# Performance work log

Hardware: AMD Instinct MI355X
Metric: run time of the kernel (lower is better)

The kernel has to match this reference:

```python
import jax, jax.numpy as jnp
import numpy as np

B_, L_, D_, H_ = 2, 1024, 1024, 16


def _matrixR(L, d_model):
    # Transformer-XL sinusoid table, reversed along the position axis (reverse=True)
    inv_freq = 1.0 / (10000.0 ** (np.arange(0, d_model, 2, dtype=np.float32) / d_model))
    sinus = np.arange(L, dtype=np.float32)[:, None] * inv_freq[None, :]
    mat = np.zeros((L, d_model), dtype=np.float32)
    mat[:, 0::2] = np.sin(sinus)
    mat[:, 1::2] = np.cos(sinus)
    return jnp.asarray(mat[::-1].copy())


def _shift_b(x):
    # x: (b, h, L, L) -> TXL relative shift + lower-triangular mask
    b, h, L, _ = x.shape
    pad = jnp.concatenate([jnp.zeros((b, h, L, 1), x.dtype), x], axis=-1)  # (b,h,L,L+1)
    shifted = pad.reshape(b, h, L + 1, L)[:, :, 1:, :]                      # (b,h,L,L)
    return jnp.tril(shifted)


def setup_inputs() -> dict:
    key = jax.random.key(0)
    ks = jax.random.split(key, 8)
    s = 1.0 / np.sqrt(D_)
    return {
        "E": jax.random.normal(ks[0], (B_, L_, D_), dtype=jnp.float32),
        "Ev": jax.random.normal(ks[1], (B_, L_, D_), dtype=jnp.float32),
        "R": _matrixR(L_, D_),
        "Wq": jax.random.normal(ks[2], (D_, D_), dtype=jnp.float32) * s,
        "Wke": jax.random.normal(ks[3], (D_, D_), dtype=jnp.float32) * s,
        "Wkr": jax.random.normal(ks[4], (D_, D_), dtype=jnp.float32) * s,
        "Wv": jax.random.normal(ks[5], (D_, D_), dtype=jnp.float32) * s,
        "cb": jnp.ones((D_,), dtype=jnp.float32),
        "pb": jnp.ones((D_,), dtype=jnp.float32),
        "Wo_w": jax.random.normal(ks[6], (D_, D_), dtype=jnp.float32) * s,
        "Wo_b": jnp.zeros((D_,), dtype=jnp.float32),
        "ln_g": jnp.ones((D_,), dtype=jnp.float32),
        "ln_b": jnp.zeros((D_,), dtype=jnp.float32),
    }


def reference(E, Ev, R, Wq, Wke, Wkr, Wv, cb, pb, Wo_w, Wo_b, ln_g, ln_b):
    b, L, d = E.shape
    h = H_
    dh = d // h
    # projections -> (b, h, L, dh)
    q = (E @ Wq).reshape(b, L, h, dh).transpose(0, 2, 1, 3)
    k = (Ev @ Wke).reshape(b, L, h, dh).transpose(0, 2, 1, 3)
    v = (Ev @ Wv).reshape(b, L, h, dh).transpose(0, 2, 1, 3)
    # relative-position keys (batch independent): (h, L, dh)
    Q = (R @ Wkr).reshape(L, h, dh).transpose(1, 0, 2)
    # (a) content-content
    A_a = jnp.einsum('bhid,bhjd->bhij', q, k)
    # (b) content-position, with shift trick
    A_b = _shift_b(jnp.einsum('bhid,hjd->bhij', q, Q))
    # (c) global content bias (same for every query row)
    A_c = jnp.einsum('hd,bhjd->bhj', cb.reshape(h, dh), k)[:, :, None, :]  # (b,h,1,L)
    # (d) global position bias (batch independent), shifted
    d_row = jnp.einsum('hd,hjd->hj', pb.reshape(h, dh), Q)                 # (h,L)
    A_d = _shift_b(jnp.broadcast_to(d_row[None, :, None, :], (1, h, L, L)))
    A = A_a + A_b + A_c + A_d
    p = jax.nn.softmax(A, axis=-1)
    Oh = jnp.einsum('bhij,bhjd->bhid', p, v)
    O = Oh.transpose(0, 2, 1, 3).reshape(b, L, d)
    # residual + output proj (dropout is identity in eval) + LayerNorm
    res = Ev + (O @ Wo_w + Wo_b)
    mu = jnp.mean(res, axis=-1, keepdims=True)
    var = jnp.mean((res - mu) ** 2, axis=-1, keepdims=True)
    return (res - mu) * jax.lax.rsqrt(var + 1e-5) * ln_g + ln_b
```

## Files before the change

kernel.cpp:

```cpp
#include <hip/hip_runtime.h>
#include <hip/hip_bf16.h>
#include <math.h>

#define B_ 2
#define L_ 1024
#define D_ 1024
#define H_ 16

typedef short short8 __attribute__((ext_vector_type(8)));
typedef short short4v __attribute__((ext_vector_type(4)));
typedef float f32x4  __attribute__((ext_vector_type(4)));

__device__ __forceinline__ short f2bf(float f) {
  unsigned u = __float_as_uint(f);
  u += 0x7fff + ((u >> 16) & 1);
  return (short)(u >> 16);
}
__device__ __forceinline__ float bf2f(short s) {
  return __uint_as_float(((unsigned)(unsigned short)s) << 16);
}
__device__ __forceinline__ int swz(int row, int slot) {
  return row * 64 + (((slot ^ row) & 7) << 3);
}
__device__ __forceinline__ int pkey(int row) {
  return (row & 7) ^ ((row & 8) >> 2);
}
__device__ __forceinline__ void glds16(const void* g, void* l) {
  __builtin_amdgcn_global_load_lds((const __attribute__((address_space(1))) void*)g,
                                   (__attribute__((address_space(3))) void*)l, 16, 0, 0);
}

__global__ __launch_bounds__(256) void prep(
    const float* __restrict__ E, const float* __restrict__ Ev,
    const float* __restrict__ R,
    const float* __restrict__ W0, const float* __restrict__ W1,
    const float* __restrict__ W2, const float* __restrict__ W3,
    const float* __restrict__ W4,
    short* __restrict__ act, short* __restrict__ Wt) {
  __shared__ short t[64][65];
  const int tid = threadIdx.x;
  int bid = blockIdx.x;
  if (bid < 2560) {
    size_t i8 = ((size_t)bid * 256 + tid) * 8;
    const float* src; size_t off;
    if (i8 < 2097152)      { src = E;  off = i8; }
    else if (i8 < 4194304) { src = Ev; off = i8 - 2097152; }
    else                   { src = R;  off = i8 - 4194304; }
    float4 a = *(const float4*)&src[off];
    float4 b = *(const float4*)&src[off + 4];
    short8 v;
    v[0] = f2bf(a.x); v[1] = f2bf(a.y); v[2] = f2bf(a.z); v[3] = f2bf(a.w);
    v[4] = f2bf(b.x); v[5] = f2bf(b.y); v[6] = f2bf(b.z); v[7] = f2bf(b.w);
    *(short8*)&act[i8] = v;
    return;
  }
  bid -= 2560;
  const int z = bid >> 8, rem = bid & 255;
  const int by = rem >> 4, bx = rem & 15;
  const float* W = (z == 0) ? W0 : (z == 1) ? W1 : (z == 2) ? W2 : (z == 3) ? W3 : W4;
  short* Wtz = Wt + (size_t)z * D_ * D_;
  const int r0 = by * 64, c0 = bx * 64;
  #pragma unroll
  for (int i = 0; i < 4; ++i) {
    int idx = tid + i * 256;
    int r = idx >> 4, c4 = (idx & 15) * 4;
    float4 v = *(const float4*)&W[(size_t)(r0 + r) * D_ + c0 + c4];
    t[c4 + 0][r] = f2bf(v.x); t[c4 + 1][r] = f2bf(v.y);
    t[c4 + 2][r] = f2bf(v.z); t[c4 + 3][r] = f2bf(v.w);
  }
  __syncthreads();
  #pragma unroll
  for (int i = 0; i < 2; ++i) {
    int idx = tid + i * 256;
    int rr = idx >> 3, cc = (idx & 7) * 8;
    short8 o;
    #pragma unroll
    for (int e = 0; e < 8; ++e) o[e] = t[rr][cc + e];
    *(short8*)&Wtz[(size_t)(c0 + rr) * D_ + r0 + cc] = o;
  }
}

template<int NF, int OUT>
__device__ __forceinline__ void mm_db(const short* __restrict__ A,
                                      const short* __restrict__ Bt,
                                      void* __restrict__ Cp,
                                      int bx, int by) {
  __shared__ short As0[4096], As1[4096];
  __shared__ short Bs0[NF * 2048], Bs1[NF * 2048];
  const int tid = threadIdx.x;
  const int l = tid & 63, w = tid >> 6;
  const int row0 = by * 64, col0 = bx * (NF * 32);
  const int wm = (w >> 1) * 32, wn = (w & 1) * (NF * 16);
  const int lr = l >> 3;
  const int lc = ((l & 7) ^ lr) * 8;
  const f32x4 fz = {0.f, 0.f, 0.f, 0.f};

  f32x4 acc[2][NF];
  #pragma unroll
  for (int i = 0; i < 2; ++i)
    #pragma unroll
    for (int j = 0; j < NF; ++j) acc[i][j] = fz;

  auto STAGE = [&](short* AsD, short* BsD, int k0) {
    #pragma unroll
    for (int c = 0; c < 2; ++c) {
      int ch = w * 2 + c;
      glds16(&A[(size_t)(row0 + ch * 8 + lr) * 1024 + k0 + lc], &AsD[ch * 512]);
    }
    #pragma unroll
    for (int c = 0; c < NF; ++c) {
      int ch = w * NF + c;
      glds16(&Bt[(size_t)(col0 + ch * 8 + lr) * 1024 + k0 + lc], &BsD[ch * 512]);
    }
  };
  auto COMP = [&](const short* AsS, const short* BsS) {
    #pragma unroll
    for (int kf = 0; kf < 2; ++kf) {
      const int slot = kf * 4 + (l >> 4);
      short8 a[2], bfr[NF];
      #pragma unroll
      for (int mf = 0; mf < 2; ++mf)
        a[mf] = *(const short8*)&AsS[swz(wm + mf * 16 + (l & 15), slot)];
      #pragma unroll
      for (int nf = 0; nf < NF; ++nf)
        bfr[nf] = *(const short8*)&BsS[swz(wn + nf * 16 + (l & 15), slot)];
      #pragma unroll
      for (int mf = 0; mf < 2; ++mf)
        #pragma unroll
        for (int nf = 0; nf < NF; ++nf)
          acc[mf][nf] = __builtin_amdgcn_mfma_f32_16x16x32_bf16(a[mf], bfr[nf], acc[mf][nf], 0, 0, 0);
    }
  };

  STAGE(As0, Bs0, 0);
  __syncthreads();
  for (int t = 0; t < 16; t += 2) {
    if (t + 1 < 16) STAGE(As1, Bs1, (t + 1) * 64);
    COMP(As0, Bs0);
    __syncthreads();
    if (t + 2 < 16) STAGE(As0, Bs0, (t + 2) * 64);
    COMP(As1, Bs1);
    __syncthreads();
  }

  #pragma unroll
  for (int mf = 0; mf < 2; ++mf)
    #pragma unroll
    for (int nf = 0; nf < NF; ++nf) {
      if (OUT == 2) {
        int tok = row0 + wm + mf * 16 + (l >> 4) * 4;
        int col = col0 + wn + nf * 16 + (l & 15);
        int bb = tok >> 10, j = tok & 1023;
        int h = col >> 6, d = col & 63;
        short4v o;
        #pragma unroll
        for (int r = 0; r < 4; ++r) o[r] = f2bf(acc[mf][nf][r]);
        *(short4v*)&((short*)Cp)[((size_t)((bb * H_ + h) * 64 + d)) * 1024 + j] = o;
      } else {
        #pragma unroll
        for (int r = 0; r < 4; ++r) {
          int row = row0 + wm + mf * 16 + (l >> 4) * 4 + r;
          int col = col0 + wn + nf * 16 + (l & 15);
          if (OUT == 1) ((float*)Cp)[(size_t)row * 1024 + col] = acc[mf][nf][r];
          else          ((short*)Cp)[(size_t)row * 1024 + col] = f2bf(acc[mf][nf][r]);
        }
      }
    }
}

__global__ __launch_bounds__(256) void proj_g(
    const short* __restrict__ Eb, const short* __restrict__ Evb,
    const short* __restrict__ Rb, const short* __restrict__ Wt,
    short* __restrict__ qb, short* __restrict__ kb,
    short* __restrict__ vt, short* __restrict__ Qpb) {
  const int z = blockIdx.z;
  const size_t MM = (size_t)D_ * D_;
  const short* A; const short* Bt; short* C; int M;
  if (z == 0)      { A = Eb;  Bt = Wt;          C = qb;  M = B_ * L_; }
  else if (z == 1) { A = Evb; Bt = Wt + MM;     C = kb;  M = B_ * L_; }
  else if (z == 2) { A = Evb; Bt = Wt + 3 * MM; C = vt;  M = B_ * L_; }
  else             { A = Rb;  Bt = Wt + 2 * MM; C = Qpb; M = L_;      }
  if ((int)blockIdx.y * 64 >= M) return;
  if (z == 2) mm_db<2, 2>(A, Bt, C, blockIdx.x, blockIdx.y);
  else        mm_db<2, 0>(A, Bt, C, blockIdx.x, blockIdx.y);
}

__global__ __launch_bounds__(256) void out_g(
    const short* __restrict__ Ob, const short* __restrict__ Wot,
    float* __restrict__ proj) {
  mm_db<2, 1>(Ob, Wot, proj, blockIdx.x, blockIdx.y);
}

__global__ __launch_bounds__(64) void attn_d(
    const short* __restrict__ qb, const short* __restrict__ kb,
    const short* __restrict__ vt, const short* __restrict__ Qpb,
    const float* __restrict__ cb, const float* __restrict__ pb,
    short* __restrict__ Ob) {
  __shared__ short pbs[1312];

  const int l = threadIdx.x & 63;
  const int hl = blockIdx.x & 31;
  const int it = blockIdx.x >> 5;
  const int b = hl >> 4, hh = hl & 15;
  const int i0 = it * 16;
  const f32x4 fz = {0.f, 0.f, 0.f, 0.f};

  short8 aqc[2], aqp[2];
  {
    const size_t qoff = (size_t)(b * L_ + i0 + (l & 15)) * D_ + hh * 64 + (l >> 4) * 8;
    #pragma unroll
    for (int kf = 0; kf < 2; ++kf) {
      short8 qv = *(const short8*)&qb[qoff + kf * 32];
      f32x4 c0 = *(const f32x4*)&cb[hh * 64 + kf * 32 + (l >> 4) * 8];
      f32x4 c1 = *(const f32x4*)&cb[hh * 64 + kf * 32 + (l >> 4) * 8 + 4];
      f32x4 p0 = *(const f32x4*)&pb[hh * 64 + kf * 32 + (l >> 4) * 8];
      f32x4 p1 = *(const f32x4*)&pb[hh * 64 + kf * 32 + (l >> 4) * 8 + 4];
      #pragma unroll
      for (int e = 0; e < 8; ++e) {
        float q = bf2f(qv[e]);
        float cc = (e < 4) ? c0[e] : c1[e - 4];
        float pp = (e < 4) ? p0[e] : p1[e - 4];
        aqc[kf][e] = f2bf(q + cc);
        aqp[kf][e] = f2bf(q + pp);
      }
    }
  }

  const short* kbase  = &kb[(size_t)(b * L_) * D_ + hh * 64 + (l >> 4) * 8];
  const short* vtbase = &vt[(size_t)((b * H_ + hh) * 64) * 1024 + (l >> 4) * 8];
  const short* wbase  = &Qpb[hh * 64 + (l >> 4) * 8];

  short8 bk[2][4], bw[2][5], bv[2][4];

  auto LK = [&](int jt) {
    const int j0 = jt * 64;
    #pragma unroll
    for (int kf = 0; kf < 2; ++kf)
      #pragma unroll
      for (int nf = 0; nf < 4; ++nf)
        bk[kf][nf] = *(const short8*)&kbase[(size_t)(j0 + nf * 16 + (l & 15)) * D_ + kf * 32];
  };
  auto LW = [&](int jt) {
    const int mb = L_ - 16 - (i0 - jt * 64);
    #pragma unroll
    for (int kf = 0; kf < 2; ++kf)
      #pragma unroll
      for (int u = 0; u < 5; ++u) {
        int m = mb + u * 16 + (l & 15);
        m = (m < L_) ? m : (L_ - 1);
        bw[kf][u] = *(const short8*)&wbase[(size_t)m * D_ + kf * 32];
      }
  };
  auto LV = [&](int jt) {
    const int j0 = jt * 64;
    #pragma unroll
    for (int kf = 0; kf < 2; ++kf)
      #pragma unroll
      for (int nf = 0; nf < 4; ++nf)
        bv[kf][nf] = *(const short8*)&vtbase[(size_t)(nf * 16 + (l & 15)) * 1024 + j0 + kf * 32];
  };

  LK(0); LW(0);

  float mrow[4], lrow[4];
  f32x4 oacc[4];
  #pragma unroll
  for (int r = 0; r < 4; ++r) { mrow[r] = -3.0e38f; lrow[r] = 0.f; }
  #pragma unroll
  for (int nf = 0; nf < 4; ++nf) oacc[nf] = fz;

  for (int jt = 0; jt < 16; ++jt) {
    const int dth = i0 - jt * 64;
    const bool pos = (dth >= -15);

    LV(jt);

    f32x4 sac[4];
    #pragma unroll
    for (int nf = 0; nf < 4; ++nf) sac[nf] = fz;
    __builtin_amdgcn_s_setprio(1);
    #pragma unroll
    for (int kf = 0; kf < 2; ++kf)
      #pragma unroll
      for (int nf = 0; nf < 4; ++nf)
        sac[nf] = __builtin_amdgcn_mfma_f32_16x16x32_bf16(aqc[kf], bk[kf][nf], sac[nf], 0, 0, 0);
    __builtin_amdgcn_s_setprio(0);

    if (pos) {
      f32x4 pacc[5];
      #pragma unroll
      for (int u = 0; u < 5; ++u) pacc[u] = fz;
      __builtin_amdgcn_s_setprio(1);
      #pragma unroll
      for (int kf = 0; kf < 2; ++kf)
        #pragma unroll
        for (int u = 0; u < 5; ++u)
          pacc[u] = __builtin_amdgcn_mfma_f32_16x16x32_bf16(aqp[kf], bw[kf][u], pacc[u], 0, 0, 0);
      __builtin_amdgcn_s_setprio(0);
      #pragma unroll
      for (int u = 0; u < 5; ++u)
        #pragma unroll
        for (int r = 0; r < 4; ++r) {
          int row = (l >> 4) * 4 + r;
          pbs[row * 82 + u * 16 + (l & 15)] = f2bf(pacc[u][r]);
        }
    }

    if (jt < 15) {
      LK(jt + 1);
      if (dth - 64 >= -15) LW(jt + 1);
    }

    if (pos) {
      #pragma unroll
      for (int nf = 0; nf < 4; ++nf)
        #pragma unroll
        for (int r = 0; r < 4; ++r) {
          int ris = (l >> 4) * 4 + r;
          int rj = nf * 16 + (l & 15);
          if (rj <= ris + dth)
            sac[nf][r] += bf2f(pbs[ris * 82 + (15 - ris + rj)]);
        }
    }

    #pragma unroll
    for (int r = 0; r < 4; ++r) {
      float mx = fmaxf(fmaxf(sac[0][r], sac[1][r]), fmaxf(sac[2][r], sac[3][r]));
      #pragma unroll
      for (int off = 1; off < 16; off <<= 1)
        mx = fmaxf(mx, __shfl_xor(mx, off, 64));
      float mn = fmaxf(mrow[r], mx);
      float sc = __expf(mrow[r] - mn);
      mrow[r] = mn;
      float ls = 0.f;
      #pragma unroll
      for (int nf = 0; nf < 4; ++nf) {
        float p = __expf(sac[nf][r] - mn);
        sac[nf][r] = p;
        ls += p;
      }
      #pragma unroll
      for (int off = 1; off < 16; off <<= 1)
        ls += __shfl_xor(ls, off, 64);
      lrow[r] = lrow[r] * sc + ls;
      #pragma unroll
      for (int nf = 0; nf < 4; ++nf) oacc[nf][r] *= sc;
    }

    #pragma unroll
    for (int nf = 0; nf < 4; ++nf)
      #pragma unroll
      for (int r = 0; r < 4; ++r) {
        int row = (l >> 4) * 4 + r;
        int col = nf * 16 + (l & 15);
        pbs[row * 64 + (((col >> 3) ^ pkey(row)) << 3) + (col & 7)] = f2bf(sac[nf][r]);
      }

    __builtin_amdgcn_s_setprio(1);
    #pragma unroll
    for (int kf = 0; kf < 2; ++kf) {
      int prow = l & 15;
      short8 ap = *(const short8*)&pbs[prow * 64 + (((kf * 4 + (l >> 4)) ^ pkey(prow)) << 3)];
      #pragma unroll
      for (int nf = 0; nf < 4; ++nf)
        oacc[nf] = __builtin_amdgcn_mfma_f32_16x16x32_bf16(ap, bv[kf][nf], oacc[nf], 0, 0, 0);
    }
    __builtin_amdgcn_s_setprio(0);
  }

  #pragma unroll
  for (int r = 0; r < 4; ++r) {
    float inv = 1.f / lrow[r];
    #pragma unroll
    for (int nf = 0; nf < 4; ++nf) {
      int row = i0 + (l >> 4) * 4 + r;
      int col = hh * 64 + nf * 16 + (l & 15);
      Ob[(size_t)(b * L_ + row) * D_ + col] = f2bf(oacc[nf][r] * inv);
    }
  }
}

__global__ __launch_bounds__(256) void ln_kernel(
    const float* __restrict__ Ev, const float* __restrict__ proj,
    const float* __restrict__ Wo_b, const float* __restrict__ g,
    const float* __restrict__ beta, float* __restrict__ out) {
  const int row = blockIdx.x;
  __shared__ float red[8];
  const int tid = threadIdx.x;
  const int d = tid * 4;

  float4 e  = *(const float4*)&Ev[(size_t)row * D_ + d];
  float4 p  = *(const float4*)&proj[(size_t)row * D_ + d];
  float4 wb = *(const float4*)&Wo_b[d];
  float4 rr = { e.x + p.x + wb.x, e.y + p.y + wb.y,
                e.z + p.z + wb.z, e.w + p.w + wb.w };
  float sum = rr.x + rr.y + rr.z + rr.w;
  float sq  = rr.x * rr.x + rr.y * rr.y + rr.z * rr.z + rr.w * rr.w;

  #pragma unroll
  for (int off = 1; off < 64; off <<= 1) {
    sum += __shfl_xor(sum, off, 64);
    sq  += __shfl_xor(sq,  off, 64);
  }
  const int wid = tid >> 6;
  if ((tid & 63) == 0) { red[wid * 2] = sum; red[wid * 2 + 1] = sq; }
  __syncthreads();
  sum = red[0] + red[2] + red[4] + red[6];
  sq  = red[1] + red[3] + red[5] + red[7];

  const float mu   = sum * (1.f / (float)D_);
  const float var  = sq * (1.f / (float)D_) - mu * mu;
  const float rstd = rsqrtf(var + 1e-5f);

  float4 gg = *(const float4*)&g[d];
  float4 bb = *(const float4*)&beta[d];
  float4 o = { (rr.x - mu) * rstd * gg.x + bb.x,
               (rr.y - mu) * rstd * gg.y + bb.y,
               (rr.z - mu) * rstd * gg.z + bb.z,
               (rr.w - mu) * rstd * gg.w + bb.w };
  *(float4*)&out[(size_t)row * D_ + d] = o;
}

extern "C" void kernel_launch(void* const* d_in, const int* in_sizes, int n_in,
                              void* d_out, int out_size, void* d_ws, size_t ws_size,
                              hipStream_t stream) {
  const float* E    = (const float*)d_in[0];
  const float* Ev   = (const float*)d_in[1];
  const float* R    = (const float*)d_in[2];
  const float* Wq   = (const float*)d_in[3];
  const float* Wke  = (const float*)d_in[4];
  const float* Wkr  = (const float*)d_in[5];
  const float* Wv   = (const float*)d_in[6];
  const float* cb   = (const float*)d_in[7];
  const float* pb   = (const float*)d_in[8];
  const float* Wo_w = (const float*)d_in[9];
  const float* Wo_b = (const float*)d_in[10];
  const float* ln_g = (const float*)d_in[11];
  const float* ln_b = (const float*)d_in[12];
  float* out = (float*)d_out;

  short* ws   = (short*)d_ws;
  short* Eb   = ws;
  short* Evb  = ws + 2097152;
  short* Rb   = ws + 4194304;
  short* qb   = ws + 5242880;
  short* kb   = ws + 7340032;
  short* vt   = ws + 9437184;
  short* Qpb  = ws + 11534336;
  short* Wt   = ws + 12582912;
  short* Ob   = ws + 17825792;
  float* proj = (float*)Eb;

  prep<<<3840, 256, 0, stream>>>(E, Ev, R, Wq, Wke, Wkr, Wv, Wo_w, Eb, Wt);

  proj_g<<<dim3(16, 32, 4), 256, 0, stream>>>(Eb, Evb, Rb, Wt, qb, kb, vt, Qpb);

  attn_d<<<2048, 64, 0, stream>>>(qb, kb, vt, Qpb, cb, pb, Ob);

  out_g<<<dim3(16, 32), 256, 0, stream>>>(Ob, Wt + 4 * (size_t)D_ * D_, proj);

  ln_kernel<<<B_ * L_, 256, 0, stream>>>(Ev, proj, Wo_b, ln_g, ln_b, out);
}
```

Before: 240.7 us.

## Share K/V tiles across four waves via double-buffered LDS in attention

The attention kernel changes from one 64-thread wave per 16-row query tile to 256-thread blocks of four waves covering 64 query rows. K and V^T tiles are staged into double-buffered shared memory with swizzled layout using direct global-to-LDS loads, and a block barrier closes each iteration. This lets four waves share each K/V tile instead of each wave reading it separately from global memory. The projection GEMM also switches to a wider tile template with half as many x-blocks. The cost is block-level synchronisation, more LDS use per block, and fewer blocks (512) in the attention launch.

```diff
diff --git a/kernel.cpp b/kernel.cpp
--- a/kernel.cpp
+++ b/kernel.cpp
@@ -181,8 +181,8 @@
   else if (z == 2) { A = Evb; Bt = Wt + 3 * MM; C = vt;  M = B_ * L_; }
   else             { A = Rb;  Bt = Wt + 2 * MM; C = Qpb; M = L_;      }
   if ((int)blockIdx.y * 64 >= M) return;
-  if (z == 2) mm_db<2, 2>(A, Bt, C, blockIdx.x, blockIdx.y);
-  else        mm_db<2, 0>(A, Bt, C, blockIdx.x, blockIdx.y);
+  if (z == 2) mm_db<4, 2>(A, Bt, C, blockIdx.x, blockIdx.y);
+  else        mm_db<4, 0>(A, Bt, C, blockIdx.x, blockIdx.y);
 }
 
 __global__ __launch_bounds__(256) void out_g(
@@ -191,57 +191,61 @@
   mm_db<2, 1>(Ob, Wot, proj, blockIdx.x, blockIdx.y);
 }
 
-__global__ __launch_bounds__(64) void attn_d(
+__global__ __launch_bounds__(256, 3) void attn_s(
     const short* __restrict__ qb, const short* __restrict__ kb,
     const short* __restrict__ vt, const short* __restrict__ Qpb,
     const float* __restrict__ cb, const float* __restrict__ pb,
     short* __restrict__ Ob) {
-  __shared__ short pbs[1312];
-
-  const int l = threadIdx.x & 63;
+  __shared__ short k_s0[4096], k_s1[4096];
+  __shared__ short vt_s0[4096], vt_s1[4096];
+  __shared__ short pbs[4 * 1312];
+
+  const int tid = threadIdx.x;
+  const int l = tid & 63, w = tid >> 6;
   const int hl = blockIdx.x & 31;
   const int it = blockIdx.x >> 5;
   const int b = hl >> 4, hh = hl & 15;
-  const int i0 = it * 16;
+  const int i0 = it * 64;
+  const int i0w = i0 + w * 16;
   const f32x4 fz = {0.f, 0.f, 0.f, 0.f};
+
+  const int lr = l >> 3;
+  const int lc = ((l & 7) ^ lr) * 8;
 
   short8 aqc[2], aqp[2];
   {
-    const size_t qoff = (size_t)(b * L_ + i0 + (l & 15)) * D_ + hh * 64 + (l >> 4) * 8;
+    const size_t qoff = (size_t)(b * L_ + i0w + (l & 15)) * D_ + hh * 64 + (l >> 4) * 8;
     #pragma unroll
     for (int kf = 0; kf < 2; ++kf) {
       short8 qv = *(const short8*)&qb[qoff + kf * 32];
-      f32x4 c0 = *(const f32x4*)&cb[hh * 64 + kf * 32 + (l >> 4) * 8];
-      f32x4 c1 = *(const f32x4*)&cb[hh * 64 + kf * 32 + (l >> 4) * 8 + 4];
-      f32x4 p0 = *(const f32x4*)&pb[hh * 64 + kf * 32 + (l >> 4) * 8];
-      f32x4 p1 = *(const f32x4*)&pb[hh * 64 + kf * 32 + (l >> 4) * 8 + 4];
+      const float* cbp = &cb[hh * 64 + kf * 32 + (l >> 4) * 8];
+      const float* pbp = &pb[hh * 64 + kf * 32 + (l >> 4) * 8];
       #pragma unroll
       for (int e = 0; e < 8; ++e) {
         float q = bf2f(qv[e]);
-        float cc = (e < 4) ? c0[e] : c1[e - 4];
-        float pp = (e < 4) ? p0[e] : p1[e - 4];
-        aqc[kf][e] = f2bf(q + cc);
-        aqp[kf][e] = f2bf(q + pp);
-      }
-    }
-  }
-
-  const short* kbase  = &kb[(size_t)(b * L_) * D_ + hh * 64 + (l >> 4) * 8];
-  const short* vtbase = &vt[(size_t)((b * H_ + hh) * 64) * 1024 + (l >> 4) * 8];
+        aqc[kf][e] = f2bf(q + cbp[e]);
+        aqp[kf][e] = f2bf(q + pbp[e]);
+      }
+    }
+  }
+
+  const short* kbase  = &kb[(size_t)(b * L_) * D_ + hh * 64];
+  const short* vtbase = &vt[(size_t)((b * H_ + hh) * 64) * 1024];
   const short* wbase  = &Qpb[hh * 64 + (l >> 4) * 8];
 
-  short8 bk[2][4], bw[2][5], bv[2][4];
-
-  auto LK = [&](int jt) {
+  auto STAGE = [&](short* kD, short* vD, int jt) {
     const int j0 = jt * 64;
     #pragma unroll
-    for (int kf = 0; kf < 2; ++kf)
-      #pragma unroll
-      for (int nf = 0; nf < 4; ++nf)
-        bk[kf][nf] = *(const short8*)&kbase[(size_t)(j0 + nf * 16 + (l & 15)) * D_ + kf * 32];
+    for (int c = 0; c < 2; ++c) {
+      int ch = w * 2 + c;
+      glds16(&kbase[(size_t)(j0 + ch * 8 + lr) * D_ + lc], &kD[ch * 512]);
+      glds16(&vtbase[(size_t)(ch * 8 + lr) * 1024 + j0 + lc], &vD[ch * 512]);
+    }
   };
+
+  short8 bw[2][5];
   auto LW = [&](int jt) {
-    const int mb = L_ - 16 - (i0 - jt * 64);
+    const int mb = L_ - 16 - (i0w - jt * 64);
     #pragma unroll
     for (int kf = 0; kf < 2; ++kf)
       #pragma unroll
@@ -251,16 +255,10 @@
         bw[kf][u] = *(const short8*)&wbase[(size_t)m * D_ + kf * 32];
       }
   };
-  auto LV = [&](int jt) {
-    const int j0 = jt * 64;
-    #pragma unroll
-    for (int kf = 0; kf < 2; ++kf)
-      #pragma unroll
-      for (int nf = 0; nf < 4; ++nf)
-        bv[kf][nf] = *(const short8*)&vtbase[(size_t)(nf * 16 + (l & 15)) * 1024 + j0 + kf * 32];
-  };
-
-  LK(0); LW(0);
+
+  STAGE(k_s0, vt_s0, 0);
+  LW(0);
+  __syncthreads();
 
   float mrow[4], lrow[4];
   f32x4 oacc[4];
@@ -269,21 +267,31 @@
   #pragma unroll
   for (int nf = 0; nf < 4; ++nf) oacc[nf] = fz;
 
+  const int pbb = w * 1312;
+
   for (int jt = 0; jt < 16; ++jt) {
-    const int dth = i0 - jt * 64;
+    const int dth = i0w - jt * 64;
     const bool pos = (dth >= -15);
-
-    LV(jt);
+    const short* kS  = (jt & 1) ? k_s1 : k_s0;
+    const short* vS  = (jt & 1) ? vt_s1 : vt_s0;
+    short* kD = (jt & 1) ? k_s0 : k_s1;
+    short* vD = (jt & 1) ? vt_s0 : vt_s1;
+
+    if (jt < 15) STAGE(kD, vD, jt + 1);
 
     f32x4 sac[4];
     #pragma unroll
     for (int nf = 0; nf < 4; ++nf) sac[nf] = fz;
     __builtin_amdgcn_s_setprio(1);
     #pragma unroll
-    for (int kf = 0; kf < 2; ++kf)
-      #pragma unroll
-      for (int nf = 0; nf < 4; ++nf)
-        sac[nf] = __builtin_amdgcn_mfma_f32_16x16x32_bf16(aqc[kf], bk[kf][nf], sac[nf], 0, 0, 0);
+    for (int kf = 0; kf < 2; ++kf) {
+      const int slot = kf * 4 + (l >> 4);
+      #pragma unroll
+      for (int nf = 0; nf < 4; ++nf) {
+        short8 bk = *(const short8*)&kS[swz(nf * 16 + (l & 15), slot)];
+        sac[nf] = __builtin_amdgcn_mfma_f32_16x16x32_bf16(aqc[kf], bk, sac[nf], 0, 0, 0);
+      }
+    }
     __builtin_amdgcn_s_setprio(0);
 
     if (pos) {
@@ -302,14 +310,11 @@
         #pragma unroll
         for (int r = 0; r < 4; ++r) {
           int row = (l >> 4) * 4 + r;
-          pbs[row * 82 + u * 16 + (l & 15)] = f2bf(pacc[u][r]);
+          pbs[pbb + row * 82 + u * 16 + (l & 15)] = f2bf(pacc[u][r]);
         }
     }
 
-    if (jt < 15) {
-      LK(jt + 1);
-      if (dth - 64 >= -15) LW(jt + 1);
-    }
+    if (jt < 15 && dth - 64 >= -15) LW(jt + 1);
 
     if (pos) {
       #pragma unroll
@@ -319,7 +324,7 @@
           int ris = (l >> 4) * 4 + r;
           int rj = nf * 16 + (l & 15);
           if (rj <= ris + dth)
-            sac[nf][r] += bf2f(pbs[ris * 82 + (15 - ris + rj)]);
+            sac[nf][r] += bf2f(pbs[pbb + ris * 82 + (15 - ris + rj)]);
         }
     }
 
@@ -353,19 +358,23 @@
       for (int r = 0; r < 4; ++r) {
         int row = (l >> 4) * 4 + r;
         int col = nf * 16 + (l & 15);
-        pbs[row * 64 + (((col >> 3) ^ pkey(row)) << 3) + (col & 7)] = f2bf(sac[nf][r]);
+        pbs[pbb + row * 64 + (((col >> 3) ^ pkey(row)) << 3) + (col & 7)] = f2bf(sac[nf][r]);
       }
 
     __builtin_amdgcn_s_setprio(1);
     #pragma unroll
     for (int kf = 0; kf < 2; ++kf) {
       int prow = l & 15;
-      short8 ap = *(const short8*)&pbs[prow * 64 + (((kf * 4 + (l >> 4)) ^ pkey(prow)) << 3)];
-      #pragma unroll
-      for (int nf = 0; nf < 4; ++nf)
-        oacc[nf] = __builtin_amdgcn_mfma_f32_16x16x32_bf16(ap, bv[kf][nf], oacc[nf], 0, 0, 0);
+      short8 ap = *(const short8*)&pbs[pbb + prow * 64 + (((kf * 4 + (l >> 4)) ^ pkey(prow)) << 3)];
+      #pragma unroll
+      for (int nf = 0; nf < 4; ++nf) {
+        short8 bv = *(const short8*)&vS[swz(nf * 16 + (l & 15), kf * 4 + (l >> 4))];
+        oacc[nf] = __builtin_amdgcn_mfma_f32_16x16x32_bf16(ap, bv, oacc[nf], 0, 0, 0);
+      }
     }
     __builtin_amdgcn_s_setprio(0);
+
+    __syncthreads();
   }
 
   #pragma unroll
@@ -373,7 +382,7 @@
     float inv = 1.f / lrow[r];
     #pragma unroll
     for (int nf = 0; nf < 4; ++nf) {
-      int row = i0 + (l >> 4) * 4 + r;
+      int row = i0w + (l >> 4) * 4 + r;
       int col = hh * 64 + nf * 16 + (l & 15);
       Ob[(size_t)(b * L_ + row) * D_ + col] = f2bf(oacc[nf][r] * inv);
     }
@@ -453,9 +462,9 @@
 
   prep<<<3840, 256, 0, stream>>>(E, Ev, R, Wq, Wke, Wkr, Wv, Wo_w, Eb, Wt);
 
-  proj_g<<<dim3(16, 32, 4), 256, 0, stream>>>(Eb, Evb, Rb, Wt, qb, kb, vt, Qpb);
-
-  attn_d<<<2048, 64, 0, stream>>>(qb, kb, vt, Qpb, cb, pb, Ob);
+  proj_g<<<dim3(8, 32, 4), 256, 0, stream>>>(Eb, Evb, Rb, Wt, qb, kb, vt, Qpb);
+
+  attn_s<<<512, 256, 0, stream>>>(qb, kb, vt, Qpb, cb, pb, Ob);
 
   out_g<<<dim3(16, 32), 256, 0, stream>>>(Ob, Wt + 4 * (size_t)D_ * D_, proj);
 
```

Result: faster. 224.0 us (-6.9%).
